# Kernel tuning notes

Measured on AMD Instinct MI355X. Metric: run time of the kernel, lower is better.

## Reference

```python
import jax, jax.numpy as jnp
import numpy as np

NUM_ITERS = 2  # quasi-DEER fixed-point iterations (module default num_iters=2)


def _affine_scan(A, b):
    """Parallel first-order linear recurrence h_t = A_t*h_{t-1} + b_t along axis=1.
    A, b: (B, T, H). Equivalent to torch accelerated-scan after removing pow-2 padding."""
    def comb(l, r):
        A1, b1 = l
        A2, b2 = r
        return A2 * A1, A2 * b1 + b2
    return jax.lax.associative_scan(comb, (A, b), axis=1)[1]


def _run_direction(x, W_in, b_in, W_rec, U_z, b_u, num_iters):
    """quasi-DEER evaluation of a MinRNN layer.
    x: (B, T, d_in). Returns states (B, T, H). Initial state h0 = 0 (hx=None)."""
    B, T, _ = x.shape
    H = b_in.shape[0]
    dtype = x.dtype
    h0 = jnp.zeros((B, H), dtype)
    diag_rec = jnp.diagonal(W_rec)  # (H,)
    # z depends only on the input, not on the state -> precompute once.
    z = jnp.tanh(jnp.einsum('bti,hi->bth', x, W_in) + b_in)  # (B, T, H)
    z0, z_rest = z[:, 0], z[:, 1:]
    states = jnp.zeros((B, T, H), dtype)
    for _ in range(num_iters):
        h_prev = states[:, :-1]  # (B, T-1, H), paired with inputs[:,1:]
        u = jax.nn.sigmoid(jnp.einsum('bth,gh->btg', h_prev, W_rec)
                           + jnp.einsum('bth,gh->btg', z_rest, U_z) + b_u)
        fs = u * h_prev + (1.0 - u) * z_rest                      # cell output f
        As = u + (h_prev - z_rest) * u * (1.0 - u) * diag_rec     # diagonal Jacobian
        bs = fs - As * h_prev
        u0 = jax.nn.sigmoid(h0 @ W_rec.T + z0 @ U_z.T + b_u)
        b0 = u0 * h0 + (1.0 - u0) * z0                            # f(x_0, h0)
        A = jnp.concatenate([jnp.zeros_like(b0)[:, None], As], axis=1)  # A0 = 0
        b = jnp.concatenate([b0[:, None], bs], axis=1)
        states = _affine_scan(A, b)
    return states


def _prnn_forward(input, Wf_in, bf_in, Wf_rec, Uf_z, bf_u,
                  Wb_in, bb_in, Wb_rec, Ub_z, bb_u):
    fwd = _run_direction(input, Wf_in, bf_in, Wf_rec, Uf_z, bf_u, NUM_ITERS)
    bwd = _run_direction(input[:, ::-1], Wb_in, bb_in, Wb_rec, Ub_z, bb_u, NUM_ITERS)[:, ::-1]
    output = jnp.concatenate([fwd, bwd], axis=2)      # (B, T, 2H)
    h_n = jnp.stack([fwd[:, -1], bwd[:, 0]])          # (2, B, H)
    return output, h_n


def setup_inputs() -> dict:
    key = jax.random.key(0)
    ks = jax.random.split(key, 12)
    B, T, D_IN, H = 8, 8192, 256, 256
    def minrnn_params(k0, k1, k2, d_in, h):
        kw, kr, ku = k0, k1, k2
        return dict(
            W_in=jax.random.normal(kw, (h, d_in), jnp.float32) / d_in ** 0.5,
            b_in=jnp.zeros((h,), jnp.float32),
            W_rec=jax.random.normal(kr, (h, h), jnp.float32) / h ** 0.5,
            U_z=jax.random.normal(ku, (h, h), jnp.float32) / h ** 0.5,
            b_u=jnp.zeros((h,), jnp.float32),
        )
    pf = minrnn_params(ks[0], ks[1], ks[2], D_IN, H)
    pb = minrnn_params(ks[3], ks[4], ks[5], D_IN, H)
    return {
        'input': jax.random.normal(ks[6], (B, T, D_IN), jnp.float32),
        'Wf_in': pf['W_in'], 'bf_in': pf['b_in'], 'Wf_rec': pf['W_rec'],
        'Uf_z': pf['U_z'], 'bf_u': pf['b_u'],
        'Wb_in': pb['W_in'], 'bb_in': pb['b_in'], 'Wb_rec': pb['W_rec'],
        'Ub_z': pb['U_z'], 'bb_u': pb['b_u'],
    }


def reference(input, Wf_in, bf_in, Wf_rec, Uf_z, bf_u,
              Wb_in, bb_in, Wb_rec, Ub_z, bb_u):
    return _prnn_forward(input, Wf_in, bf_in, Wf_rec, Uf_z, bf_u,
                         Wb_in, bb_in, Wb_rec, Ub_z, bb_u)
```

## Files before the change

kernel.cpp:

```cpp
#include <hip/hip_runtime.h>
#include <stdint.h>

typedef unsigned short u16;
typedef __attribute__((ext_vector_type(8))) short short8v;
typedef __attribute__((ext_vector_type(4))) short short4v;
typedef __attribute__((ext_vector_type(4))) float f32x4;

#define B_ 8
#define T_ 8192
#define H_ 256
#define M_ 65536
#define MH 16777216
#define NCH 256
#define CHL 32
#define NCHAN 4096

__device__ __forceinline__ u16 f2bf(float f) {
  union { float f; uint32_t u; } v; v.f = f;
  return (u16)((v.u + 0x7FFFu + ((v.u >> 16) & 1u)) >> 16);
}
__device__ __forceinline__ float bf2f(u16 s) {
  union { uint32_t u; float f; } v; v.u = ((uint32_t)s) << 16;
  return v.f;
}
__device__ __forceinline__ float sigm(float x) {
  return __fdividef(1.0f, 1.0f + __expf(-x));
}
__device__ __forceinline__ float tanhfast(float x) {
  return 1.0f - __fdividef(2.0f, __expf(2.0f * x) + 1.0f);
}

__global__ __launch_bounds__(256) void cvt_x_kernel(const float* __restrict__ x,
                                                    u16* __restrict__ xf) {
  size_t i = ((size_t)blockIdx.x * 256 + threadIdx.x) * 8;
  const float4* src = (const float4*)(x + i);
  float4 a = src[0], b = src[1];
  short8v o;
  o[0] = (short)f2bf(a.x); o[1] = (short)f2bf(a.y);
  o[2] = (short)f2bf(a.z); o[3] = (short)f2bf(a.w);
  o[4] = (short)f2bf(b.x); o[5] = (short)f2bf(b.y);
  o[6] = (short)f2bf(b.z); o[7] = (short)f2bf(b.w);
  *(short8v*)(xf + i) = o;
}

__global__ __launch_bounds__(256) void cvt_w_kernel(const float* __restrict__ s0, const float* __restrict__ s1,
                                                    const float* __restrict__ s2, const float* __restrict__ s3,
                                                    const float* __restrict__ s4, const float* __restrict__ s5,
                                                    u16* __restrict__ wbf) {
  int i = blockIdx.x * 256 + threadIdx.x;
  int m = i >> 16, r = i & 65535;
  const float* s = (m == 0) ? s0 : (m == 1) ? s1 : (m == 2) ? s2 : (m == 3) ? s3 : (m == 4) ? s4 : s5;
  wbf[i] = f2bf(s[r]);
}

__device__ __forceinline__ void g2l16(const void* g, void* l) {
  __builtin_amdgcn_global_load_lds((const __attribute__((address_space(1))) void*)g,
                                   (__attribute__((address_space(3))) void*)l, 16, 0, 0);
}

template <int EPI, int REV>
__global__ __launch_bounds__(256) void gemm_k(const u16* __restrict__ A,
                                              const u16* __restrict__ Bw,
                                              const float* __restrict__ bias,
                                              const u16* addm,
                                              u16* C) {
  __shared__ __align__(16) char ldsA[16384];
  __shared__ __align__(16) char ldsB[16384];
  const int tid = threadIdx.x;
  const int l = tid & 63, w = tid >> 6;
  const int tm = blockIdx.x, tn = blockIdx.y;
  const int m0 = (w >> 1) * 64, n0 = (w & 1) * 64;
  const int wbase = w * 1024;

  f32x4 vzero = {0.f, 0.f, 0.f, 0.f};
  f32x4 acc[4][4];
#pragma unroll
  for (int i = 0; i < 4; ++i)
#pragma unroll
    for (int j = 0; j < 4; ++j) acc[i][j] = vzero;

#pragma unroll
  for (int k0 = 0; k0 < 256; k0 += 64) {
#pragma unroll
    for (int is = 0; is < 4; ++is) {
      const int o = is * 4096 + tid * 16;
      const int row = o >> 7;
      const int cb = o & 127;
      int rA = tm * 128 + row;
      if (REV) { int bb = rA >> 13; int t = rA & 8191; rA = (bb << 13) + (8191 - t); }
      const char* gA = (const char*)A + (size_t)rA * 512 + k0 * 2 + cb;
      g2l16(gA, ldsA + is * 4096 + wbase);
      const int rB = tn * 128 + row;
      const char* gB = (const char*)Bw + (size_t)rB * 512 + k0 * 2 + cb;
      g2l16(gB, ldsB + is * 4096 + wbase);
    }
    __syncthreads();
#pragma unroll
    for (int ks = 0; ks < 2; ++ks) {
      short8v av[4], bv[4];
#pragma unroll
      for (int i = 0; i < 4; ++i) {
        av[i] = *(const short8v*)(ldsA + (m0 + i * 16 + (l & 15)) * 128 + ks * 64 + (l >> 4) * 16);
        bv[i] = *(const short8v*)(ldsB + (n0 + i * 16 + (l & 15)) * 128 + ks * 64 + (l >> 4) * 16);
      }
#pragma unroll
      for (int i = 0; i < 4; ++i)
#pragma unroll
        for (int j = 0; j < 4; ++j)
          acc[i][j] = __builtin_amdgcn_mfma_f32_16x16x32_bf16(av[i], bv[j], acc[i][j], 0, 0, 0);
    }
    __syncthreads();
  }

  const int colb = tn * 128 + n0 + (l & 15);
  const int rowb = tm * 128 + m0 + ((l >> 4) << 2);
#pragma unroll
  for (int j = 0; j < 4; ++j) {
    const int col = colb + j * 16;
    const float bv = (EPI == 3) ? 0.f : bias[col];
#pragma unroll
    for (int i = 0; i < 4; ++i)
#pragma unroll
      for (int r = 0; r < 4; ++r) {
        const int row = rowb + i * 16 + r;
        float xv = acc[i][j][r] + bv;
        if (EPI == 3) xv += bf2f(addm[(size_t)row * 256 + col]);
        if (EPI == 0) xv = tanhfast(xv);
        C[(size_t)row * 256 + col] = f2bf(xv);
      }
  }
}

__device__ __forceinline__ void compute_Ab(float zf, float ag, float hp, float dr,
                                           float& Aa, float& bb) {
  const float u = sigm(ag);
  const float g = u * (1.f - u) * dr;
  Aa = u + (hp - zf) * g;
  bb = u * hp + (1.f - u) * zf - Aa * hp;
}

template <int ITER>
__global__ __launch_bounds__(256) void scan_p1_kernel(
    const u16* __restrict__ zb, const u16* __restrict__ zub,
    const u16* __restrict__ s1b,
    const float* __restrict__ Wf_rec, const float* __restrict__ Wb_rec,
    float* __restrict__ P, float* __restrict__ q) {
  const int wid = blockIdx.x * 4 + (threadIdx.x >> 6);
  const int lane = threadIdx.x & 63;
  const int c = wid & (NCH - 1);
  const int tmp = wid >> 8;
  const int b = tmp & 7;
  const int d = tmp >> 3;
  const int h0 = lane * 4;
  const float* Wr = d ? Wb_rec : Wf_rec;
  float dr[4];
#pragma unroll
  for (int j = 0; j < 4; ++j) dr[j] = Wr[(h0 + j) * 257];
  const size_t off = (size_t)d * MH + ((size_t)b * T_ + (size_t)c * CHL) * H_ + h0;
  const u16* zp = zb + off;
  const u16* zup = zub + off;
  const u16* s1p = s1b + off;
  float Pv[4] = {1.f, 1.f, 1.f, 1.f}, qv[4] = {0.f, 0.f, 0.f, 0.f};
#pragma unroll 4
  for (int it = 0; it < CHL; ++it) {
    const size_t ix = (size_t)it * H_;
    short4v z4 = *(const short4v*)(zp + ix);
    short4v a4 = *(const short4v*)(zup + ix);
    short4v s4 = {0, 0, 0, 0};
    if (ITER == 2) s4 = *(const short4v*)(s1p + ix);
#pragma unroll
    for (int j = 0; j < 4; ++j) {
      const float zf = bf2f((u16)z4[j]);
      const float ag = bf2f((u16)a4[j]);
      const float hp = (ITER == 2) ? bf2f((u16)s4[j]) : 0.f;
      float Aa, bb;
      compute_Ab(zf, ag, hp, dr[j], Aa, bb);
      qv[j] = Aa * qv[j] + bb;
      Pv[j] *= Aa;
    }
  }
  const int ch0 = (d * 8 + b) * 256 + h0;
  *(f32x4*)(P + (size_t)c * NCHAN + ch0) = (f32x4){Pv[0], Pv[1], Pv[2], Pv[3]};
  *(f32x4*)(q + (size_t)c * NCHAN + ch0) = (f32x4){qv[0], qv[1], qv[2], qv[3]};
}

__global__ __launch_bounds__(256) void scan_p2_kernel(const float* __restrict__ P,
                                                      const float* __restrict__ q,
                                                      float* __restrict__ hstart) {
  const int ch = blockIdx.x * 256 + threadIdx.x;
  float hs = 0.f;
#pragma unroll 8
  for (int c = 0; c < NCH; ++c) {
    hstart[c * NCHAN + ch] = hs;
    hs = P[c * NCHAN + ch] * hs + q[c * NCHAN + ch];
  }
}

template <int ITER>
__global__ __launch_bounds__(256) void scan_p3_kernel(
    const u16* __restrict__ zb, const u16* __restrict__ zub,
    const u16* __restrict__ s1b,
    const float* __restrict__ Wf_rec, const float* __restrict__ Wb_rec,
    const float* __restrict__ hstart,
    u16* __restrict__ s1out, float* __restrict__ out, float* __restrict__ hn) {
  const int wid = blockIdx.x * 4 + (threadIdx.x >> 6);
  const int lane = threadIdx.x & 63;
  const int c = wid & (NCH - 1);
  const int tmp = wid >> 8;
  const int b = tmp & 7;
  const int d = tmp >> 3;
  const int h0 = lane * 4;
  const float* Wr = d ? Wb_rec : Wf_rec;
  float dr[4];
#pragma unroll
  for (int j = 0; j < 4; ++j) dr[j] = Wr[(h0 + j) * 257];
  const size_t off = (size_t)d * MH + ((size_t)b * T_ + (size_t)c * CHL) * H_ + h0;
  const u16* zp = zb + off;
  const u16* zup = zub + off;
  const u16* s1p = s1b + off;
  const int ch0 = (d * 8 + b) * 256 + h0;
  f32x4 h4 = *(const f32x4*)(hstart + (size_t)c * NCHAN + ch0);
  float hc[4] = {h4[0], h4[1], h4[2], h4[3]};
  if (ITER == 1 && c == 0) {
    *(short4v*)(s1out + off) = (short4v){0, 0, 0, 0};
  }
#pragma unroll 4
  for (int it = 0; it < CHL; ++it) {
    const size_t ix = (size_t)it * H_;
    short4v z4 = *(const short4v*)(zp + ix);
    short4v a4 = *(const short4v*)(zup + ix);
    short4v s4 = {0, 0, 0, 0};
    if (ITER == 2) s4 = *(const short4v*)(s1p + ix);
#pragma unroll
    for (int j = 0; j < 4; ++j) {
      const float zf = bf2f((u16)z4[j]);
      const float ag = bf2f((u16)a4[j]);
      const float hp = (ITER == 2) ? bf2f((u16)s4[j]) : 0.f;
      float Aa, bb;
      compute_Ab(zf, ag, hp, dr[j], Aa, bb);
      hc[j] = Aa * hc[j] + bb;
    }
    const int t = c * CHL + it;
    if (ITER == 1) {
      if (t < T_ - 1) {
        short4v o = {(short)f2bf(hc[0]), (short)f2bf(hc[1]),
                     (short)f2bf(hc[2]), (short)f2bf(hc[3])};
        *(short4v*)(s1out + off + ix + H_) = o;
      }
    } else {
      const size_t to = (d == 0) ? ((size_t)b * T_ + t) * 512 + h0
                                 : ((size_t)b * T_ + (T_ - 1 - t)) * 512 + 256 + h0;
      *(f32x4*)(out + to) = (f32x4){hc[0], hc[1], hc[2], hc[3]};
      if (t == T_ - 1)
        *(f32x4*)(hn + (size_t)(d * 8 + b) * 256 + h0) = (f32x4){hc[0], hc[1], hc[2], hc[3]};
    }
  }
}

extern "C" void kernel_launch(void* const* d_in, const int* in_sizes, int n_in,
                              void* d_out, int out_size, void* d_ws, size_t ws_size,
                              hipStream_t stream) {
  const float* x      = (const float*)d_in[0];
  const float* Wf_in  = (const float*)d_in[1];
  const float* bf_in  = (const float*)d_in[2];
  const float* Wf_rec = (const float*)d_in[3];
  const float* Uf_z   = (const float*)d_in[4];
  const float* bf_u   = (const float*)d_in[5];
  const float* Wb_in  = (const float*)d_in[6];
  const float* bb_in  = (const float*)d_in[7];
  const float* Wb_rec = (const float*)d_in[8];
  const float* Ub_z   = (const float*)d_in[9];
  const float* bb_u   = (const float*)d_in[10];

  char* ws = (char*)d_ws;
  const size_t BF = 33554432;
  u16* xf  = (u16*)(ws + 0 * BF);
  u16* z0  = (u16*)(ws + 1 * BF);
  u16* z1  = (u16*)(ws + 2 * BF);
  u16* zu0 = (u16*)(ws + 3 * BF);
  u16* zu1 = (u16*)(ws + 4 * BF);
  u16* s10 = (u16*)(ws + 5 * BF);
  u16* s11 = (u16*)(ws + 6 * BF);
  u16* wbf    = (u16*)(ws + 7 * BF);
  float* Pbuf = (float*)(ws + 7 * BF + 786432);
  float* qbuf = (float*)(ws + 7 * BF + 786432 + 4194304);
  float* hst  = (float*)(ws + 7 * BF + 786432 + 8388608);
  (void)ws_size; (void)in_sizes; (void)n_in; (void)out_size;

  float* outp = (float*)d_out;
  float* hnp  = outp + (size_t)33554432;

  dim3 gg(512, 2, 1);

  cvt_x_kernel<<<8192, 256, 0, stream>>>(x, xf);
  cvt_w_kernel<<<1536, 256, 0, stream>>>(Wf_in, Uf_z, Wf_rec, Wb_in, Ub_z, Wb_rec, wbf);

  gemm_k<0, 0><<<gg, 256, 0, stream>>>(xf, wbf + 0 * 65536, bf_in, nullptr, z0);
  gemm_k<0, 1><<<gg, 256, 0, stream>>>(xf, wbf + 3 * 65536, bb_in, nullptr, z1);
  gemm_k<1, 0><<<gg, 256, 0, stream>>>(z0, wbf + 1 * 65536, bf_u, nullptr, zu0);
  gemm_k<1, 0><<<gg, 256, 0, stream>>>(z1, wbf + 4 * 65536, bb_u, nullptr, zu1);

  scan_p1_kernel<1><<<1024, 256, 0, stream>>>(z0, zu0, s10, Wf_rec, Wb_rec, Pbuf, qbuf);
  scan_p2_kernel<<<16, 256, 0, stream>>>(Pbuf, qbuf, hst);
  scan_p3_kernel<1><<<1024, 256, 0, stream>>>(z0, zu0, s10, Wf_rec, Wb_rec, hst,
                                              s10, nullptr, nullptr);

  gemm_k<3, 0><<<gg, 256, 0, stream>>>(s10, wbf + 2 * 65536, nullptr, zu0, zu0);
  gemm_k<3, 0><<<gg, 256, 0, stream>>>(s11, wbf + 5 * 65536, nullptr, zu1, zu1);

  scan_p1_kernel<2><<<1024, 256, 0, stream>>>(z0, zu0, s10, Wf_rec, Wb_rec, Pbuf, qbuf);
  scan_p2_kernel<<<16, 256, 0, stream>>>(Pbuf, qbuf, hst);
  scan_p3_kernel<2><<<1024, 256, 0, stream>>>(z0, zu0, s10, Wf_rec, Wb_rec, hst,
                                              nullptr, outp, hnp);
}
```

Baseline: 404.3 us.

## Fuse three-pass scan into single-pass decoupled lookback, batch GEMMs, stage epilogue via LDS

Replaces the three scan kernels (chunk reduce, serial carry pass, chunk rescan) with one kernel per iteration. Each wave publishes its chunk aggregate, then gets its carry-in by a decoupled lookback over flag-guarded aggregates. This removes the serial carry kernel and one full re-read of the inputs. It also merges the forward and backward GEMMs into one launch via blockIdx.z, fuses the conversion kernels and flag clearing into a single prep launch, and writes GEMM outputs through LDS for coalesced 16-byte stores. The cost is spin-waiting on flags, which relies on earlier chunks' waves being scheduled ahead, and chunk length doubles to 64.

```diff
diff --git a/kernel.cpp b/kernel.cpp
--- a/kernel.cpp
+++ b/kernel.cpp
@@ -11,9 +11,10 @@
 #define H_ 256
 #define M_ 65536
 #define MH 16777216
-#define NCH 256
-#define CHL 32
-#define NCHAN 4096
+#define NCH 128
+#define CHL 64
+#define NSEQ 16
+#define NS 2048
 
 __device__ __forceinline__ u16 f2bf(float f) {
   union { float f; uint32_t u; } v; v.f = f;
@@ -30,27 +31,41 @@
   return 1.0f - __fdividef(2.0f, __expf(2.0f * x) + 1.0f);
 }
 
-__global__ __launch_bounds__(256) void cvt_x_kernel(const float* __restrict__ x,
-                                                    u16* __restrict__ xf) {
-  size_t i = ((size_t)blockIdx.x * 256 + threadIdx.x) * 8;
-  const float4* src = (const float4*)(x + i);
-  float4 a = src[0], b = src[1];
-  short8v o;
-  o[0] = (short)f2bf(a.x); o[1] = (short)f2bf(a.y);
-  o[2] = (short)f2bf(a.z); o[3] = (short)f2bf(a.w);
-  o[4] = (short)f2bf(b.x); o[5] = (short)f2bf(b.y);
-  o[6] = (short)f2bf(b.z); o[7] = (short)f2bf(b.w);
-  *(short8v*)(xf + i) = o;
-}
-
-__global__ __launch_bounds__(256) void cvt_w_kernel(const float* __restrict__ s0, const float* __restrict__ s1,
-                                                    const float* __restrict__ s2, const float* __restrict__ s3,
-                                                    const float* __restrict__ s4, const float* __restrict__ s5,
-                                                    u16* __restrict__ wbf) {
-  int i = blockIdx.x * 256 + threadIdx.x;
-  int m = i >> 16, r = i & 65535;
-  const float* s = (m == 0) ? s0 : (m == 1) ? s1 : (m == 2) ? s2 : (m == 3) ? s3 : (m == 4) ? s4 : s5;
-  wbf[i] = f2bf(s[r]);
+__global__ __launch_bounds__(256) void prep_kernel(
+    const float* __restrict__ x, u16* __restrict__ xf,
+    const float* __restrict__ w0, const float* __restrict__ w1, const float* __restrict__ w2,
+    const float* __restrict__ w3, const float* __restrict__ w4, const float* __restrict__ w5,
+    u16* __restrict__ wbf, int* __restrict__ flags) {
+  const int bx = blockIdx.x;
+  if (bx < 8192) {
+    size_t i = ((size_t)bx * 256 + threadIdx.x) * 8;
+    const float4* src = (const float4*)(x + i);
+    float4 a = src[0], b = src[1];
+    short8v o;
+    o[0] = (short)f2bf(a.x); o[1] = (short)f2bf(a.y);
+    o[2] = (short)f2bf(a.z); o[3] = (short)f2bf(a.w);
+    o[4] = (short)f2bf(b.x); o[5] = (short)f2bf(b.y);
+    o[6] = (short)f2bf(b.z); o[7] = (short)f2bf(b.w);
+    *(short8v*)(xf + i) = o;
+  } else if (bx < 8384) {
+    const int r = bx - 8192;
+    const int wsel = r >> 5, blk = r & 31;
+    const float* s = (wsel == 0) ? w0 : (wsel == 1) ? w1 : (wsel == 2) ? w2
+                   : (wsel == 3) ? w3 : (wsel == 4) ? w4 : w5;
+    size_t i = ((size_t)blk * 256 + threadIdx.x) * 8;
+    const float4* src = (const float4*)(s + i);
+    float4 a = src[0], b = src[1];
+    short8v o;
+    o[0] = (short)f2bf(a.x); o[1] = (short)f2bf(a.y);
+    o[2] = (short)f2bf(a.z); o[3] = (short)f2bf(a.w);
+    o[4] = (short)f2bf(b.x); o[5] = (short)f2bf(b.y);
+    o[6] = (short)f2bf(b.z); o[7] = (short)f2bf(b.w);
+    *(short8v*)(wbf + (size_t)wsel * 65536 + i) = o;
+  } else {
+    int4* f4 = (int4*)flags;
+#pragma unroll
+    for (int k = 0; k < 4; ++k) f4[k * 256 + threadIdx.x] = (int4){0, 0, 0, 0};
+  }
 }
 
 __device__ __forceinline__ void g2l16(const void* g, void* l) {
@@ -58,19 +73,28 @@
                                    (__attribute__((address_space(3))) void*)l, 16, 0, 0);
 }
 
-template <int EPI, int REV>
-__global__ __launch_bounds__(256) void gemm_k(const u16* __restrict__ A,
+template <int EPI, int REVZ>
+__global__ __launch_bounds__(256) void gemm_k(const u16* __restrict__ A, size_t strideA,
                                               const u16* __restrict__ Bw,
-                                              const float* __restrict__ bias,
-                                              const u16* addm,
-                                              u16* C) {
-  __shared__ __align__(16) char ldsA[16384];
-  __shared__ __align__(16) char ldsB[16384];
+                                              const float* __restrict__ bias0,
+                                              const float* __restrict__ bias1,
+                                              const u16* addm, u16* C) {
+  __shared__ __align__(16) char lds[32768];
+  char* ldsA = lds;
+  char* ldsB = lds + 16384;
+  const int bz = blockIdx.z;
+  A += (size_t)bz * strideA;
+  Bw += (size_t)bz * 196608;
+  C += (size_t)bz * (size_t)MH;
+  if (EPI == 3) addm += (size_t)bz * (size_t)MH;
+  const float* bias = bz ? bias1 : bias0;
+
   const int tid = threadIdx.x;
   const int l = tid & 63, w = tid >> 6;
   const int tm = blockIdx.x, tn = blockIdx.y;
   const int m0 = (w >> 1) * 64, n0 = (w & 1) * 64;
   const int wbase = w * 1024;
+  const bool rev = REVZ && (bz == 1);
 
   f32x4 vzero = {0.f, 0.f, 0.f, 0.f};
   f32x4 acc[4][4];
@@ -87,7 +111,7 @@
       const int row = o >> 7;
       const int cb = o & 127;
       int rA = tm * 128 + row;
-      if (REV) { int bb = rA >> 13; int t = rA & 8191; rA = (bb << 13) + (8191 - t); }
+      if (rev) { int bb = rA >> 13; int t = rA & 8191; rA = (bb << 13) + (8191 - t); }
       const char* gA = (const char*)A + (size_t)rA * 512 + k0 * 2 + cb;
       g2l16(gA, ldsA + is * 4096 + wbase);
       const int rB = tn * 128 + row;
@@ -112,22 +136,32 @@
     __syncthreads();
   }
 
-  const int colb = tn * 128 + n0 + (l & 15);
-  const int rowb = tm * 128 + m0 + ((l >> 4) << 2);
+  u16* lt = (u16*)lds;
+  const int colL = n0 + (l & 15);
+  const int rowL0 = m0 + ((l >> 4) << 2);
 #pragma unroll
   for (int j = 0; j < 4; ++j) {
-    const int col = colb + j * 16;
-    const float bv = (EPI == 3) ? 0.f : bias[col];
+    const int cl = colL + j * 16;
+    const int cg = tn * 128 + cl;
+    const float bv = (EPI == 3) ? 0.f : bias[cg];
 #pragma unroll
     for (int i = 0; i < 4; ++i)
 #pragma unroll
       for (int r = 0; r < 4; ++r) {
-        const int row = rowb + i * 16 + r;
+        const int rl = rowL0 + i * 16 + r;
         float xv = acc[i][j][r] + bv;
-        if (EPI == 3) xv += bf2f(addm[(size_t)row * 256 + col]);
+        if (EPI == 3) xv += bf2f(addm[(size_t)(tm * 128 + rl) * 256 + cg]);
         if (EPI == 0) xv = tanhfast(xv);
-        C[(size_t)row * 256 + col] = f2bf(xv);
-      }
+        lt[rl * 128 + cl] = f2bf(xv);
+      }
+  }
+  __syncthreads();
+#pragma unroll
+  for (int itr = 0; itr < 8; ++itr) {
+    const int rl = w * 32 + itr * 4 + (l >> 4);
+    const int cb = (l & 15) * 16;
+    short8v v = *(const short8v*)((const char*)lt + rl * 256 + cb);
+    *(short8v*)((char*)C + (size_t)(tm * 128 + rl) * 512 + tn * 256 + cb) = v;
   }
 }
 
@@ -140,17 +174,19 @@
 }
 
 template <int ITER>
-__global__ __launch_bounds__(256) void scan_p1_kernel(
+__global__ __launch_bounds__(256) void scan_kernel(
     const u16* __restrict__ zb, const u16* __restrict__ zub,
     const u16* __restrict__ s1b,
     const float* __restrict__ Wf_rec, const float* __restrict__ Wb_rec,
-    float* __restrict__ P, float* __restrict__ q) {
+    float* __restrict__ pubP, float* __restrict__ pubq,
+    float* __restrict__ inclq, int* __restrict__ flags,
+    u16* __restrict__ s1out, float* __restrict__ out, float* __restrict__ hn) {
   const int wid = blockIdx.x * 4 + (threadIdx.x >> 6);
   const int lane = threadIdx.x & 63;
   const int c = wid & (NCH - 1);
-  const int tmp = wid >> 8;
-  const int b = tmp & 7;
-  const int d = tmp >> 3;
+  const int seq = wid >> 7;
+  const int b = seq & 7;
+  const int d = seq >> 3;
   const int h0 = lane * 4;
   const float* Wr = d ? Wb_rec : Wf_rec;
   float dr[4];
@@ -160,6 +196,7 @@
   const u16* zp = zb + off;
   const u16* zup = zub + off;
   const u16* s1p = s1b + off;
+
   float Pv[4] = {1.f, 1.f, 1.f, 1.f}, qv[4] = {0.f, 0.f, 0.f, 0.f};
 #pragma unroll 4
   for (int it = 0; it < CHL; ++it) {
@@ -179,48 +216,64 @@
       Pv[j] *= Aa;
     }
   }
-  const int ch0 = (d * 8 + b) * 256 + h0;
-  *(f32x4*)(P + (size_t)c * NCHAN + ch0) = (f32x4){Pv[0], Pv[1], Pv[2], Pv[3]};
-  *(f32x4*)(q + (size_t)c * NCHAN + ch0) = (f32x4){qv[0], qv[1], qv[2], qv[3]};
-}
-
-__global__ __launch_bounds__(256) void scan_p2_kernel(const float* __restrict__ P,
-                                                      const float* __restrict__ q,
-                                                      float* __restrict__ hstart) {
-  const int ch = blockIdx.x * 256 + threadIdx.x;
-  float hs = 0.f;
-#pragma unroll 8
-  for (int c = 0; c < NCH; ++c) {
-    hstart[c * NCHAN + ch] = hs;
-    hs = P[c * NCHAN + ch] * hs + q[c * NCHAN + ch];
-  }
-}
-
-template <int ITER>
-__global__ __launch_bounds__(256) void scan_p3_kernel(
-    const u16* __restrict__ zb, const u16* __restrict__ zub,
-    const u16* __restrict__ s1b,
-    const float* __restrict__ Wf_rec, const float* __restrict__ Wb_rec,
-    const float* __restrict__ hstart,
-    u16* __restrict__ s1out, float* __restrict__ out, float* __restrict__ hn) {
-  const int wid = blockIdx.x * 4 + (threadIdx.x >> 6);
-  const int lane = threadIdx.x & 63;
-  const int c = wid & (NCH - 1);
-  const int tmp = wid >> 8;
-  const int b = tmp & 7;
-  const int d = tmp >> 3;
-  const int h0 = lane * 4;
-  const float* Wr = d ? Wb_rec : Wf_rec;
-  float dr[4];
-#pragma unroll
-  for (int j = 0; j < 4; ++j) dr[j] = Wr[(h0 + j) * 257];
-  const size_t off = (size_t)d * MH + ((size_t)b * T_ + (size_t)c * CHL) * H_ + h0;
-  const u16* zp = zb + off;
-  const u16* zup = zub + off;
-  const u16* s1p = s1b + off;
-  const int ch0 = (d * 8 + b) * 256 + h0;
-  f32x4 h4 = *(const f32x4*)(hstart + (size_t)c * NCHAN + ch0);
-  float hc[4] = {h4[0], h4[1], h4[2], h4[3]};
+
+  const size_t ps = (size_t)wid * 256 + h0;
+  if (c > 0) {
+    *(f32x4*)(pubP + ps) = (f32x4){Pv[0], Pv[1], Pv[2], Pv[3]};
+    *(f32x4*)(pubq + ps) = (f32x4){qv[0], qv[1], qv[2], qv[3]};
+    if (lane == 0)
+      __hip_atomic_store(&flags[wid], 1, __ATOMIC_RELEASE, __HIP_MEMORY_SCOPE_AGENT);
+  }
+
+  float hs[4] = {0.f, 0.f, 0.f, 0.f};
+  if (c > 0) {
+    float Pb[4] = {1.f, 1.f, 1.f, 1.f}, qb[4] = {0.f, 0.f, 0.f, 0.f};
+    const int fb = seq * NCH;
+    int j = c - 1;
+    bool done = false;
+    while (!done) {
+      const int nb = (j + 1 < 8) ? (j + 1) : 8;
+      int f[8];
+      while (true) {
+        bool ok = true;
+        for (int k = 0; k < nb; ++k) {
+          f[k] = __hip_atomic_load(&flags[fb + j - k], __ATOMIC_ACQUIRE, __HIP_MEMORY_SCOPE_AGENT);
+          ok &= (f[k] != 0);
+        }
+        if (ok) break;
+        __builtin_amdgcn_s_sleep(2);
+      }
+      for (int k = 0; k < nb && !done; ++k) {
+        const size_t js = (size_t)(fb + j - k) * 256 + h0;
+        if (f[k] == 2) {
+          f32x4 iq = *(const f32x4*)(inclq + js);
+#pragma unroll
+          for (int jj = 0; jj < 4; ++jj) hs[jj] = Pb[jj] * iq[jj] + qb[jj];
+          done = true;
+        } else {
+          f32x4 Pj = *(const f32x4*)(pubP + js);
+          f32x4 qj = *(const f32x4*)(pubq + js);
+#pragma unroll
+          for (int jj = 0; jj < 4; ++jj) {
+            qb[jj] = Pb[jj] * qj[jj] + qb[jj];
+            Pb[jj] *= Pj[jj];
+          }
+        }
+      }
+      j -= nb;
+    }
+  }
+
+  if (c < NCH - 1) {
+    f32x4 hi;
+#pragma unroll
+    for (int jj = 0; jj < 4; ++jj) hi[jj] = Pv[jj] * hs[jj] + qv[jj];
+    *(f32x4*)(inclq + ps) = hi;
+    if (lane == 0)
+      __hip_atomic_store(&flags[wid], 2, __ATOMIC_RELEASE, __HIP_MEMORY_SCOPE_AGENT);
+  }
+
+  float hc[4] = {hs[0], hs[1], hs[2], hs[3]};
   if (ITER == 1 && c == 0) {
     *(short4v*)(s1out + off) = (short4v){0, 0, 0, 0};
   }
@@ -276,40 +329,38 @@
   const size_t BF = 33554432;
   u16* xf  = (u16*)(ws + 0 * BF);
   u16* z0  = (u16*)(ws + 1 * BF);
-  u16* z1  = (u16*)(ws + 2 * BF);
   u16* zu0 = (u16*)(ws + 3 * BF);
-  u16* zu1 = (u16*)(ws + 4 * BF);
   u16* s10 = (u16*)(ws + 5 * BF);
-  u16* s11 = (u16*)(ws + 6 * BF);
-  u16* wbf    = (u16*)(ws + 7 * BF);
-  float* Pbuf = (float*)(ws + 7 * BF + 786432);
-  float* qbuf = (float*)(ws + 7 * BF + 786432 + 4194304);
-  float* hst  = (float*)(ws + 7 * BF + 786432 + 8388608);
+  u16* wbf = (u16*)(ws + 7 * BF);
+  char* pb = ws + 7 * BF + 1048576;
+  float* pubP1  = (float*)(pb);
+  float* pubq1  = (float*)(pb + 2097152);
+  float* inclq1 = (float*)(pb + 2 * 2097152);
+  float* pubP2  = (float*)(pb + 3 * 2097152);
+  float* pubq2  = (float*)(pb + 4 * 2097152);
+  float* inclq2 = (float*)(pb + 5 * 2097152);
+  int*   flags  = (int*)(pb + 6 * 2097152);
+  int*   flags2 = flags + NS;
   (void)ws_size; (void)in_sizes; (void)n_in; (void)out_size;
 
   float* outp = (float*)d_out;
   float* hnp  = outp + (size_t)33554432;
 
-  dim3 gg(512, 2, 1);
-
-  cvt_x_kernel<<<8192, 256, 0, stream>>>(x, xf);
-  cvt_w_kernel<<<1536, 256, 0, stream>>>(Wf_in, Uf_z, Wf_rec, Wb_in, Ub_z, Wb_rec, wbf);
-
-  gemm_k<0, 0><<<gg, 256, 0, stream>>>(xf, wbf + 0 * 65536, bf_in, nullptr, z0);
-  gemm_k<0, 1><<<gg, 256, 0, stream>>>(xf, wbf + 3 * 65536, bb_in, nullptr, z1);
-  gemm_k<1, 0><<<gg, 256, 0, stream>>>(z0, wbf + 1 * 65536, bf_u, nullptr, zu0);
-  gemm_k<1, 0><<<gg, 256, 0, stream>>>(z1, wbf + 4 * 65536, bb_u, nullptr, zu1);
-
-  scan_p1_kernel<1><<<1024, 256, 0, stream>>>(z0, zu0, s10, Wf_rec, Wb_rec, Pbuf, qbuf);
-  scan_p2_kernel<<<16, 256, 0, stream>>>(Pbuf, qbuf, hst);
-  scan_p3_kernel<1><<<1024, 256, 0, stream>>>(z0, zu0, s10, Wf_rec, Wb_rec, hst,
-                                              s10, nullptr, nullptr);
-
-  gemm_k<3, 0><<<gg, 256, 0, stream>>>(s10, wbf + 2 * 65536, nullptr, zu0, zu0);
-  gemm_k<3, 0><<<gg, 256, 0, stream>>>(s11, wbf + 5 * 65536, nullptr, zu1, zu1);
-
-  scan_p1_kernel<2><<<1024, 256, 0, stream>>>(z0, zu0, s10, Wf_rec, Wb_rec, Pbuf, qbuf);
-  scan_p2_kernel<<<16, 256, 0, stream>>>(Pbuf, qbuf, hst);
-  scan_p3_kernel<2><<<1024, 256, 0, stream>>>(z0, zu0, s10, Wf_rec, Wb_rec, hst,
-                                              nullptr, outp, hnp);
-}
+  dim3 gg(512, 2, 2);
+
+  prep_kernel<<<8385, 256, 0, stream>>>(x, xf, Wf_in, Uf_z, Wf_rec, Wb_in, Ub_z, Wb_rec,
+                                        wbf, flags);
+
+  gemm_k<0, 1><<<gg, 256, 0, stream>>>(xf, 0, wbf + 0 * 65536, bf_in, bb_in, nullptr, z0);
+  gemm_k<1, 0><<<gg, 256, 0, stream>>>(z0, MH, wbf + 1 * 65536, bf_u, bb_u, nullptr, zu0);
+
+  scan_kernel<1><<<512, 256, 0, stream>>>(z0, zu0, s10, Wf_rec, Wb_rec,
+                                          pubP1, pubq1, inclq1, flags,
+                                          s10, nullptr, nullptr);
+
+  gemm_k<3, 0><<<gg, 256, 0, stream>>>(s10, MH, wbf + 2 * 65536, nullptr, nullptr, zu0, zu0);
+
+  scan_kernel<2><<<512, 256, 0, stream>>>(z0, zu0, s10, Wf_rec, Wb_rec,
+                                          pubP2, pubq2, inclq2, flags2,
+                                          nullptr, outp, hnp);
+}
```

Result: slower. 1.425 ms (+252.4%).

## Merge direction GEMMs via grid z, fuse conversions, stage GEMM stores through LDS

Applied to the files above, without the earlier changes.

Merges the two conversion kernels into one prep kernel that also vectorizes the weight conversion. Each pair of forward/backward GEMMs becomes a single launch using blockIdx.z to pick direction, weights, bias and buffer offsets, with the time reversal applied only for z=1. The GEMM epilogue now writes bf16 results into LDS and then emits coalesced 16-byte row stores, replacing scattered 2-byte global writes. This cuts launch count, gives each GEMM launch a larger grid, and improves store coalescing, at the cost of an extra LDS round trip and a barrier in the epilogue.

```diff
diff --git a/kernel.cpp b/kernel.cpp
--- a/kernel.cpp
+++ b/kernel.cpp
@@ -30,27 +30,34 @@
   return 1.0f - __fdividef(2.0f, __expf(2.0f * x) + 1.0f);
 }
 
-__global__ __launch_bounds__(256) void cvt_x_kernel(const float* __restrict__ x,
-                                                    u16* __restrict__ xf) {
-  size_t i = ((size_t)blockIdx.x * 256 + threadIdx.x) * 8;
-  const float4* src = (const float4*)(x + i);
-  float4 a = src[0], b = src[1];
+__global__ __launch_bounds__(256) void prep_kernel(
+    const float* __restrict__ x, u16* __restrict__ xf,
+    const float* __restrict__ w0, const float* __restrict__ w1, const float* __restrict__ w2,
+    const float* __restrict__ w3, const float* __restrict__ w4, const float* __restrict__ w5,
+    u16* __restrict__ wbf) {
+  const int bx = blockIdx.x;
+  const float* src;
+  u16* dst;
+  size_t i;
+  if (bx < 8192) {
+    i = ((size_t)bx * 256 + threadIdx.x) * 8;
+    src = x; dst = xf;
+  } else {
+    const int r = bx - 8192;
+    const int wsel = r >> 5, blk = r & 31;
+    src = (wsel == 0) ? w0 : (wsel == 1) ? w1 : (wsel == 2) ? w2
+        : (wsel == 3) ? w3 : (wsel == 4) ? w4 : w5;
+    dst = wbf + (size_t)wsel * 65536;
+    i = ((size_t)blk * 256 + threadIdx.x) * 8;
+  }
+  const float4* s4 = (const float4*)(src + i);
+  float4 a = s4[0], b = s4[1];
   short8v o;
   o[0] = (short)f2bf(a.x); o[1] = (short)f2bf(a.y);
   o[2] = (short)f2bf(a.z); o[3] = (short)f2bf(a.w);
   o[4] = (short)f2bf(b.x); o[5] = (short)f2bf(b.y);
   o[6] = (short)f2bf(b.z); o[7] = (short)f2bf(b.w);
-  *(short8v*)(xf + i) = o;
-}
-
-__global__ __launch_bounds__(256) void cvt_w_kernel(const float* __restrict__ s0, const float* __restrict__ s1,
-                                                    const float* __restrict__ s2, const float* __restrict__ s3,
-                                                    const float* __restrict__ s4, const float* __restrict__ s5,
-                                                    u16* __restrict__ wbf) {
-  int i = blockIdx.x * 256 + threadIdx.x;
-  int m = i >> 16, r = i & 65535;
-  const float* s = (m == 0) ? s0 : (m == 1) ? s1 : (m == 2) ? s2 : (m == 3) ? s3 : (m == 4) ? s4 : s5;
-  wbf[i] = f2bf(s[r]);
+  *(short8v*)(dst + i) = o;
 }
 
 __device__ __forceinline__ void g2l16(const void* g, void* l) {
@@ -58,19 +65,28 @@
                                    (__attribute__((address_space(3))) void*)l, 16, 0, 0);
 }
 
-template <int EPI, int REV>
-__global__ __launch_bounds__(256) void gemm_k(const u16* __restrict__ A,
+template <int EPI, int REVZ>
+__global__ __launch_bounds__(256) void gemm_k(const u16* __restrict__ A, size_t strideA,
                                               const u16* __restrict__ Bw,
-                                              const float* __restrict__ bias,
-                                              const u16* addm,
-                                              u16* C) {
-  __shared__ __align__(16) char ldsA[16384];
-  __shared__ __align__(16) char ldsB[16384];
+                                              const float* __restrict__ bias0,
+                                              const float* __restrict__ bias1,
+                                              const u16* addm, u16* C) {
+  __shared__ __align__(16) char lds[32768];
+  char* ldsA = lds;
+  char* ldsB = lds + 16384;
+  const int bz = blockIdx.z;
+  A += (size_t)bz * strideA;
+  Bw += (size_t)bz * 196608;
+  C += (size_t)bz * (size_t)MH;
+  if (EPI == 3) addm += (size_t)bz * (size_t)MH;
+  const float* bias = bz ? bias1 : bias0;
+
   const int tid = threadIdx.x;
   const int l = tid & 63, w = tid >> 6;
   const int tm = blockIdx.x, tn = blockIdx.y;
   const int m0 = (w >> 1) * 64, n0 = (w & 1) * 64;
   const int wbase = w * 1024;
+  const bool rev = REVZ && (bz == 1);
 
   f32x4 vzero = {0.f, 0.f, 0.f, 0.f};
   f32x4 acc[4][4];
@@ -87,7 +103,7 @@
       const int row = o >> 7;
       const int cb = o & 127;
       int rA = tm * 128 + row;
-      if (REV) { int bb = rA >> 13; int t = rA & 8191; rA = (bb << 13) + (8191 - t); }
+      if (rev) { int bb = rA >> 13; int t = rA & 8191; rA = (bb << 13) + (8191 - t); }
       const char* gA = (const char*)A + (size_t)rA * 512 + k0 * 2 + cb;
       g2l16(gA, ldsA + is * 4096 + wbase);
       const int rB = tn * 128 + row;
@@ -112,22 +128,32 @@
     __syncthreads();
   }
 
-  const int colb = tn * 128 + n0 + (l & 15);
-  const int rowb = tm * 128 + m0 + ((l >> 4) << 2);
+  u16* lt = (u16*)lds;
+  const int colL = n0 + (l & 15);
+  const int rowL0 = m0 + ((l >> 4) << 2);
 #pragma unroll
   for (int j = 0; j < 4; ++j) {
-    const int col = colb + j * 16;
-    const float bv = (EPI == 3) ? 0.f : bias[col];
+    const int cl = colL + j * 16;
+    const int cg = tn * 128 + cl;
+    const float bv = (EPI == 3) ? 0.f : bias[cg];
 #pragma unroll
     for (int i = 0; i < 4; ++i)
 #pragma unroll
       for (int r = 0; r < 4; ++r) {
-        const int row = rowb + i * 16 + r;
+        const int rl = rowL0 + i * 16 + r;
         float xv = acc[i][j][r] + bv;
-        if (EPI == 3) xv += bf2f(addm[(size_t)row * 256 + col]);
+        if (EPI == 3) xv += bf2f(addm[(size_t)(tm * 128 + rl) * 256 + cg]);
         if (EPI == 0) xv = tanhfast(xv);
-        C[(size_t)row * 256 + col] = f2bf(xv);
+        lt[rl * 128 + cl] = f2bf(xv);
       }
+  }
+  __syncthreads();
+#pragma unroll
+  for (int itr = 0; itr < 8; ++itr) {
+    const int rl = w * 32 + itr * 4 + (l >> 4);
+    const int cb = (l & 15) * 16;
+    short8v v = *(const short8v*)((const char*)lt + rl * 256 + cb);
+    *(short8v*)((char*)C + (size_t)(tm * 128 + rl) * 512 + tn * 256 + cb) = v;
   }
 }
 
@@ -276,37 +302,31 @@
   const size_t BF = 33554432;
   u16* xf  = (u16*)(ws + 0 * BF);
   u16* z0  = (u16*)(ws + 1 * BF);
-  u16* z1  = (u16*)(ws + 2 * BF);
   u16* zu0 = (u16*)(ws + 3 * BF);
-  u16* zu1 = (u16*)(ws + 4 * BF);
   u16* s10 = (u16*)(ws + 5 * BF);
-  u16* s11 = (u16*)(ws + 6 * BF);
-  u16* wbf    = (u16*)(ws + 7 * BF);
-  float* Pbuf = (float*)(ws + 7 * BF + 786432);
-  float* qbuf = (float*)(ws + 7 * BF + 786432 + 4194304);
-  float* hst  = (float*)(ws + 7 * BF + 786432 + 8388608);
+  u16* wbf = (u16*)(ws + 7 * BF);
+  char* pb = ws + 7 * BF + 1048576;
+  float* Pbuf = (float*)(pb);
+  float* qbuf = (float*)(pb + 4194304);
+  float* hst  = (float*)(pb + 8388608);
   (void)ws_size; (void)in_sizes; (void)n_in; (void)out_size;
 
   float* outp = (float*)d_out;
   float* hnp  = outp + (size_t)33554432;
 
-  dim3 gg(512, 2, 1);
-
-  cvt_x_kernel<<<8192, 256, 0, stream>>>(x, xf);
-  cvt_w_kernel<<<1536, 256, 0, stream>>>(Wf_in, Uf_z, Wf_rec, Wb_in, Ub_z, Wb_rec, wbf);
-
-  gemm_k<0, 0><<<gg, 256, 0, stream>>>(xf, wbf + 0 * 65536, bf_in, nullptr, z0);
-  gemm_k<0, 1><<<gg, 256, 0, stream>>>(xf, wbf + 3 * 65536, bb_in, nullptr, z1);
-  gemm_k<1, 0><<<gg, 256, 0, stream>>>(z0, wbf + 1 * 65536, bf_u, nullptr, zu0);
-  gemm_k<1, 0><<<gg, 256, 0, stream>>>(z1, wbf + 4 * 65536, bb_u, nullptr, zu1);
+  dim3 gg(512, 2, 2);
+
+  prep_kernel<<<8384, 256, 0, stream>>>(x, xf, Wf_in, Uf_z, Wf_rec, Wb_in, Ub_z, Wb_rec, wbf);
+
+  gemm_k<0, 1><<<gg, 256, 0, stream>>>(xf, 0, wbf + 0 * 65536, bf_in, bb_in, nullptr, z0);
+  gemm_k<1, 0><<<gg, 256, 0, stream>>>(z0, MH, wbf + 1 * 65536, bf_u, bb_u, nullptr, zu0);
 
   scan_p1_kernel<1><<<1024, 256, 0, stream>>>(z0, zu0, s10, Wf_rec, Wb_rec, Pbuf, qbuf);
   scan_p2_kernel<<<16, 256, 0, stream>>>(Pbuf, qbuf, hst);
   scan_p3_kernel<1><<<1024, 256, 0, stream>>>(z0, zu0, s10, Wf_rec, Wb_rec, hst,
                                               s10, nullptr, nullptr);
 
-  gemm_k<3, 0><<<gg, 256, 0, stream>>>(s10, wbf + 2 * 65536, nullptr, zu0, zu0);
-  gemm_k<3, 0><<<gg, 256, 0, stream>>>(s11, wbf + 5 * 65536, nullptr, zu1, zu1);
+  gemm_k<3, 0><<<gg, 256, 0, stream>>>(s10, MH, wbf + 2 * 65536, nullptr, nullptr, zu0, zu0);
 
   scan_p1_kernel<2><<<1024, 256, 0, stream>>>(z0, zu0, s10, Wf_rec, Wb_rec, Pbuf, qbuf);
   scan_p2_kernel<<<16, 256, 0, stream>>>(Pbuf, qbuf, hst);
```

Result: faster. 372.8 us (-7.8%).
